# Kernel tuning notes

Hardware: AMD Instinct MI355X
Metric: run time of the kernel (lower is better)

The kernel has to match this reference:

```python
import jax, jax.numpy as jnp
import numpy as np

N = 100000   # nodes
E = 1600000  # edges
D = 64       # input_size
H = 64       # hidden_size
OUT = 32     # output_size
HOR = 12     # horizon


def setup_inputs() -> dict:
    key = jax.random.key(0)
    ks = jax.random.split(key, 9)
    x = jax.random.normal(ks[0], (N, D), jnp.float32)
    edge_index = jax.random.randint(ks[1], (2, E), 0, N, dtype=jnp.int32)
    edge_weight = jax.random.uniform(ks[2], (E,), jnp.float32)
    s = 0.1
    W1 = jax.random.normal(ks[3], (D, H), jnp.float32) * s   # GCNConv 1 weight (no bias)
    W2 = jax.random.normal(ks[4], (H, H), jnp.float32) * s   # GCNConv 2 weight (no bias)
    A1 = jax.random.normal(ks[5], (H, H), jnp.float32) * s   # readout Linear 1
    b1 = jax.random.normal(ks[6], (H,), jnp.float32) * s
    A2 = jax.random.normal(ks[7], (H, OUT * HOR), jnp.float32) * s  # readout Linear 2
    b2 = jax.random.normal(ks[8], (OUT * HOR,), jnp.float32) * s
    return {"x": x, "edge_index": edge_index, "edge_weight": edge_weight,
            "W1": W1, "W2": W2, "A1": A1, "b1": b1, "A2": A2, "b2": b2}


def _gcn_layer(h, W, row, col, ew, n):
    # h: [n, in], W: [in, out]. PyG GCNConv: transform then symmetric-normalized aggregate.
    h = h @ W
    deg = jax.ops.segment_sum(ew, col, num_segments=n)          # degree at target nodes
    dinv = jnp.where(deg > 0, jax.lax.rsqrt(deg), 0.0)
    norm = dinv[row] * ew * dinv[col]                           # [e]
    msg = h[row] * norm[:, None]                                # gather sources, weight
    return jax.ops.segment_sum(msg, col, num_segments=n)        # scatter-add at targets


def reference(x, edge_index, edge_weight, W1, W2, A1, b1, A2, b2):
    n = x.shape[0]
    loop = jnp.arange(n, dtype=edge_index.dtype)
    row = jnp.concatenate([edge_index[0], loop])                # self-loops, weight 1
    col = jnp.concatenate([edge_index[1], loop])
    ew = jnp.concatenate([edge_weight, jnp.ones((n,), edge_weight.dtype)])
    h = jax.nn.relu(_gcn_layer(x, W1, row, col, ew, n))
    h = jax.nn.relu(_gcn_layer(h, W2, row, col, ew, n))
    # readout MLP + unflatten to [n, horizon, output_size]
    r = jax.nn.relu(h @ A1 + b1) @ A2 + b2
    r = r.reshape(n, HOR, OUT)
    return (r, h)
```

## Files before the change

kernel.cpp:

```cpp
#include <hip/hip_runtime.h>


typedef unsigned long long ull;


template <bool BUCKET>
__global__ void aggregate_kernel(const float* __restrict__ hin, float* __restrict__ hout,
                                 const int* __restrict__ meta,
                                 const int2* __restrict__ ent,
                                 const float* __restrict__ dinv, int n) {
    int gid = blockIdx.x * blockDim.x + threadIdx.x;
    int node = __builtin_amdgcn_readfirstlane(gid >> 6);
    int lane = threadIdx.x & 63;
    if (node >= n) return;
    float di = dinv[node];
    float acc0 = hin[(size_t)node * 64 + lane] * (di * di);
    float acc1 = 0.0f;
    int b, c;
    if (BUCKET) { b = node << 6; c = meta[node]; if (c > 64) c = 64; }
    else        { b = meta[node]; c = meta[node + 1] - b; }
    int e = b, end = b + c;
    for (; e + 2 <= end; e += 2) {
        int2 p0 = ent[e];
        int2 p1 = ent[e + 1];
        acc0 = fmaf(__int_as_float(p0.y), hin[(size_t)p0.x * 64 + lane], acc0);
        acc1 = fmaf(__int_as_float(p1.y), hin[(size_t)p1.x * 64 + lane], acc1);
    }
    if (e < end) {
        int2 p0 = ent[e];
        acc0 = fmaf(__int_as_float(p0.y), hin[(size_t)p0.x * 64 + lane], acc0);
    }
    hout[(size_t)node * 64 + lane] = fmaxf(acc0 + acc1, 0.0f);
}

template <bool BIAS, bool RELU>
__global__ void transform_kernel(const float* __restrict__ A, const float* __restrict__ W,
                                 const float* __restrict__ bias, float* __restrict__ out,
                                 int n, int ldw, int ldo) {
    __shared__ float Wl[64 * 64];
    int t = threadIdx.x;
    int coff = blockIdx.y * 64;
    for (int i = t; i < 4096; i += 256) {
        int k = i >> 6, c = i & 63;
        Wl[i] = W[k * ldw + coff + c];
    }
    __syncthreads();
    int wv = t >> 6, lane = t & 63;
    int row0 = (blockIdx.x * 4 + wv) * 16;
    row0 = __builtin_amdgcn_readfirstlane(row0);
    if (row0 >= n) return;
    float bv = BIAS ? bias[coff + lane] : 0.0f;
    float acc[16];
#pragma unroll
    for (int i = 0; i < 16; i++) acc[i] = bv;
    const float* Ar = A + (size_t)row0 * 64;
    int nrows = n - row0;
    if (nrows > 16) nrows = 16;
    if (nrows == 16) {
        for (int k0 = 0; k0 < 64; k0 += 4) {
            float w0 = Wl[(k0 + 0) * 64 + lane];
            float w1 = Wl[(k0 + 1) * 64 + lane];
            float w2 = Wl[(k0 + 2) * 64 + lane];
            float w3 = Wl[(k0 + 3) * 64 + lane];
#pragma unroll
            for (int i = 0; i < 16; i++) {
                float4 a = *(const float4*)(Ar + i * 64 + k0);
                acc[i] = fmaf(a.x, w0, fmaf(a.y, w1, fmaf(a.z, w2, fmaf(a.w, w3, acc[i]))));
            }
        }
#pragma unroll
        for (int i = 0; i < 16; i++) {
            float v = acc[i];
            if (RELU) v = fmaxf(v, 0.0f);
            out[(size_t)(row0 + i) * ldo + coff + lane] = v;
        }
    } else {
        for (int k = 0; k < 64; k++) {
            float w = Wl[k * 64 + lane];
            for (int i = 0; i < nrows; i++) acc[i] = fmaf(Ar[i * 64 + k], w, acc[i]);
        }
        for (int i = 0; i < nrows; i++) {
            float v = acc[i];
            if (RELU) v = fmaxf(v, 0.0f);
            out[(size_t)(row0 + i) * ldo + coff + lane] = v;
        }
    }
}

__global__ void readout_kernel(const float* __restrict__ H, const float* __restrict__ A1,
                               const float* __restrict__ b1, const float* __restrict__ A2,
                               const float* __restrict__ b2, float* __restrict__ out, int n) {
    __shared__ float Wl[64 * 64];
    __shared__ float Ml[64 * 64];
    int t = threadIdx.x;
    int wv = t >> 6, lane = t & 63;
    int wrow = blockIdx.x * 64 + wv * 16;
    wrow = __builtin_amdgcn_readfirstlane(wrow);
    int nr = n - wrow;
    if (nr > 16) nr = 16;
    if (nr < 0) nr = 0;

    for (int i = t; i < 4096; i += 256) Wl[i] = A1[i];
    __syncthreads();

    float acc[16];
    float bv = b1[lane];
#pragma unroll
    for (int i = 0; i < 16; i++) acc[i] = bv;
    const float* Ar = H + (size_t)wrow * 64;
    if (nr == 16) {
        for (int k0 = 0; k0 < 64; k0 += 4) {
            float w0 = Wl[(k0 + 0) * 64 + lane];
            float w1 = Wl[(k0 + 1) * 64 + lane];
            float w2 = Wl[(k0 + 2) * 64 + lane];
            float w3 = Wl[(k0 + 3) * 64 + lane];
#pragma unroll
            for (int i = 0; i < 16; i++) {
                float4 a = *(const float4*)(Ar + i * 64 + k0);
                acc[i] = fmaf(a.x, w0, fmaf(a.y, w1, fmaf(a.z, w2, fmaf(a.w, w3, acc[i]))));
            }
        }
    } else if (nr > 0) {
        for (int k = 0; k < 64; k++) {
            float w = Wl[k * 64 + lane];
            for (int i = 0; i < nr; i++) acc[i] = fmaf(Ar[i * 64 + k], w, acc[i]);
        }
    }
#pragma unroll
    for (int i = 0; i < 16; i++)
        Ml[(wv * 16 + i) * 64 + lane] = fmaxf(acc[i], 0.0f);

    for (int tile = 0; tile < 6; tile++) {
        int coff = tile * 64;
        __syncthreads();
        for (int i = t; i < 4096; i += 256) {
            int k = i >> 6, c = i & 63;
            Wl[i] = A2[k * 384 + coff + c];
        }
        __syncthreads();
        float bv2 = b2[coff + lane];
        float o[16];
#pragma unroll
        for (int i = 0; i < 16; i++) o[i] = bv2;
        const float* Mr = Ml + (size_t)wv * 16 * 64;
        for (int k0 = 0; k0 < 64; k0 += 4) {
            float w0 = Wl[(k0 + 0) * 64 + lane];
            float w1 = Wl[(k0 + 1) * 64 + lane];
            float w2 = Wl[(k0 + 2) * 64 + lane];
            float w3 = Wl[(k0 + 3) * 64 + lane];
#pragma unroll
            for (int i = 0; i < 16; i++) {
                float4 a = *(const float4*)(Mr + i * 64 + k0);
                o[i] = fmaf(a.x, w0, fmaf(a.y, w1, fmaf(a.z, w2, fmaf(a.w, w3, o[i]))));
            }
        }
        for (int i = 0; i < nr; i++)
            out[(size_t)(wrow + i) * 384 + coff + lane] = o[i];
    }
}


__global__ void init_cnt(int* cnt, int n) {
    int i = blockIdx.x * 256 + threadIdx.x;
    if (i < n) cnt[i] = 0;
}

__global__ void bfill_kernel(const int* __restrict__ row, const int* __restrict__ col,
                             const float* __restrict__ ew, int* cnt, int2* __restrict__ bucket,
                             int E) {
    int e = blockIdx.x * 256 + threadIdx.x;
    if (e < E) {
        int t = col[e];
        int p = atomicAdd(&cnt[t], 1);
        if (p < 64) bucket[((size_t)t << 6) + p] = make_int2(row[e], __float_as_int(ew[e]));
    }
}

__global__ void bdinv_kernel(const int* __restrict__ cnt, const int2* __restrict__ bucket,
                             float* __restrict__ dinv, int n) {
    int gid = blockIdx.x * blockDim.x + threadIdx.x;
    int node = gid >> 6;
    int lane = threadIdx.x & 63;
    if (node >= n) return;
    int c = cnt[node]; if (c > 64) c = 64;
    float w = (lane < c) ? __int_as_float(bucket[((size_t)node << 6) + lane].y) : 0.0f;
    for (int m = 32; m; m >>= 1) w += __shfl_xor(w, m, 64);
    if (lane == 0) dinv[node] = rsqrtf(1.0f + w);
}

__global__ void bnorm_kernel(const int* __restrict__ cnt, int2* bucket,
                             const float* __restrict__ dinv, int n) {
    int gid = blockIdx.x * blockDim.x + threadIdx.x;
    int node = gid >> 6;
    int slot = threadIdx.x & 63;
    if (node >= n) return;
    int c = cnt[node]; if (c > 64) c = 64;
    if (slot < c) {
        size_t idx = ((size_t)node << 6) + slot;
        int2 p = bucket[idx];
        float w = dinv[p.x] * __int_as_float(p.y) * dinv[node];
        bucket[idx].y = __float_as_int(w);
    }
}


__global__ void init_dc(ull* dc, int n) {
    int i = blockIdx.x * 256 + threadIdx.x;
    if (i < n) dc[i] = 0ull;
}

__global__ void hist_packed(const int* __restrict__ col, const float* __restrict__ ew,
                            ull* dc, int E) {
    int e = blockIdx.x * 256 + threadIdx.x;
    if (e < E) {
        int t = col[e];
        ull v = (1ull << 32) | (unsigned)lrintf(ew[e] * 1048576.0f);
        atomicAdd(&dc[t], v);
    }
}

__global__ void unpack_kernel(const ull* __restrict__ dc, int* __restrict__ cnt,
                              float* __restrict__ dinv, int n) {
    int i = blockIdx.x * 256 + threadIdx.x;
    if (i < n) {
        ull v = dc[i];
        cnt[i] = (int)(v >> 32);
        dinv[i] = rsqrtf(1.0f + (float)(unsigned)v * (1.0f / 1048576.0f));
    }
}

__global__ void scan1(const int* __restrict__ cnt, int* __restrict__ excl,
                      int* __restrict__ bsum, int n) {
    __shared__ int lds[256];
    int t = threadIdx.x;
    int idx = blockIdx.x * 1024 + t * 4;
    int4 c = make_int4(0, 0, 0, 0);
    if (idx < n) c = *(const int4*)(cnt + idx);
    int s = c.x + c.y + c.z + c.w;
    lds[t] = s;
    __syncthreads();
    for (int off = 1; off < 256; off <<= 1) {
        int u = (t >= off) ? lds[t - off] : 0;
        __syncthreads();
        lds[t] += u;
        __syncthreads();
    }
    int incl = lds[t];
    if (t == 255) bsum[blockIdx.x] = incl;
    int e0 = incl - s;
    if (idx < n) {
        excl[idx + 0] = e0;
        excl[idx + 1] = e0 + c.x;
        excl[idx + 2] = e0 + c.x + c.y;
        excl[idx + 3] = e0 + c.x + c.y + c.z;
    }
}

__global__ void scan2(int* bsum, int nb) {
    __shared__ int lds[256];
    int t = threadIdx.x;
    int v = (t < nb) ? bsum[t] : 0;
    lds[t] = v;
    __syncthreads();
    for (int off = 1; off < 256; off <<= 1) {
        int u = (t >= off) ? lds[t - off] : 0;
        __syncthreads();
        lds[t] += u;
        __syncthreads();
    }
    if (t < nb) bsum[t] = lds[t] - v;
}

__global__ void scan3(int* __restrict__ ptr, const int* __restrict__ bsum,
                      int* __restrict__ pfill, int n, int E) {
    int i = blockIdx.x * 256 + threadIdx.x;
    if (i < n) {
        int v = ptr[i] + bsum[i >> 10];
        ptr[i] = v;
        pfill[i] = v;
    }
    if (i == n) ptr[n] = E;
}

__global__ void fill_kernel(const int* __restrict__ row, const int* __restrict__ col,
                            const float* __restrict__ ew, const float* __restrict__ dinv,
                            int* pfill, int2* __restrict__ ent, int E) {
    int e = blockIdx.x * 256 + threadIdx.x;
    if (e < E) {
        int t = col[e], s = row[e];
        int p = atomicAdd(&pfill[t], 1);
        ent[p] = make_int2(s, __float_as_int(dinv[s] * ew[e] * dinv[t]));
    }
}


extern "C" void kernel_launch(void* const* d_in, const int* in_sizes, int n_in,
                              void* d_out, int out_size, void* d_ws, size_t ws_size,
                              hipStream_t stream) {
    const float* x  = (const float*)d_in[0];
    const int*   ei = (const int*)d_in[1];
    const float* ew = (const float*)d_in[2];
    const float* W1 = (const float*)d_in[3];
    const float* W2 = (const float*)d_in[4];
    const float* A1 = (const float*)d_in[5];
    const float* b1 = (const float*)d_in[6];
    const float* A2 = (const float*)d_in[7];
    const float* b2 = (const float*)d_in[8];
    float* out = (float*)d_out;

    const int N = in_sizes[0] / 64;
    const int E = in_sizes[2];
    const int* row = ei;
    const int* col = ei + E;

    float* r_out = out;
    float* h_out = out + (size_t)N * 384;

    dim3 tgrid((N + 63) / 64, 1);
    int rblocks = (N + 63) / 64;
    int aggblocks = (int)(((size_t)N * 64 + 255) / 256);
    int nblk = (N + 255) / 256;
    int eblk = (E + 255) / 256;

    char* p = (char*)d_ws;
    auto alloc = [&](size_t bytes) { void* r = (void*)p; p += (bytes + 255) & ~(size_t)255; return r; };

    size_t need_bucket = 256 * 8 + (size_t)N * 4 * 2 + ((size_t)N << 6) * 8 + (size_t)N * 64 * 4 * 2
                       + 64 * 1024;
    if (ws_size >= need_bucket) {
        int*   cnt    = (int*)alloc((size_t)N * 4);
        float* dinv   = (float*)alloc((size_t)N * 4);
        int2*  bucket = (int2*)alloc(((size_t)N << 6) * 8);
        float* h1     = (float*)alloc((size_t)N * 64 * 4);
        float* h2b    = (float*)alloc((size_t)N * 64 * 4);

        init_cnt<<<nblk, 256, 0, stream>>>(cnt, N);
        bfill_kernel<<<eblk, 256, 0, stream>>>(row, col, ew, cnt, bucket, E);
        bdinv_kernel<<<aggblocks, 256, 0, stream>>>(cnt, bucket, dinv, N);
        bnorm_kernel<<<aggblocks, 256, 0, stream>>>(cnt, bucket, dinv, N);

        transform_kernel<false, false><<<tgrid, 256, 0, stream>>>(x, W1, nullptr, h1, N, 64, 64);
        aggregate_kernel<true><<<aggblocks, 256, 0, stream>>>(h1, h2b, cnt, bucket, dinv, N);
        transform_kernel<false, false><<<tgrid, 256, 0, stream>>>(h2b, W2, nullptr, h1, N, 64, 64);
        aggregate_kernel<true><<<aggblocks, 256, 0, stream>>>(h1, h_out, cnt, bucket, dinv, N);
        readout_kernel<<<rblocks, 256, 0, stream>>>(h_out, A1, b1, A2, b2, r_out, N);
    } else {
        ull*   dc   = (ull*)alloc((size_t)N * 8);
        int*   cnt  = (int*)alloc((size_t)N * 4);
        float* dinv = (float*)alloc((size_t)N * 4);
        int*   ptr  = (int*)alloc((size_t)(N + 1) * 4);
        int*   bsum = (int*)alloc(1024);
        int2*  ent  = (int2*)alloc((size_t)E * 8);
        float* h1   = (float*)alloc((size_t)N * 64 * 4);
        float* h2b  = (float*)alloc((size_t)N * 64 * 4);
        int*   pfill = cnt;
        int nb = (N + 1023) / 1024;

        init_dc<<<nblk, 256, 0, stream>>>(dc, N);
        hist_packed<<<eblk, 256, 0, stream>>>(col, ew, dc, E);
        unpack_kernel<<<nblk, 256, 0, stream>>>(dc, cnt, dinv, N);
        scan1<<<nb, 256, 0, stream>>>(cnt, ptr, bsum, N);
        scan2<<<1, 256, 0, stream>>>(bsum, nb);
        scan3<<<(N + 256) / 256, 256, 0, stream>>>(ptr, bsum, pfill, N, E);
        fill_kernel<<<eblk, 256, 0, stream>>>(row, col, ew, dinv, pfill, ent, E);

        transform_kernel<false, false><<<tgrid, 256, 0, stream>>>(x, W1, nullptr, h1, N, 64, 64);
        aggregate_kernel<false><<<aggblocks, 256, 0, stream>>>(h1, h2b, ptr, ent, dinv, N);
        transform_kernel<false, false><<<tgrid, 256, 0, stream>>>(h2b, W2, nullptr, h1, N, 64, 64);
        aggregate_kernel<false><<<aggblocks, 256, 0, stream>>>(h1, h_out, ptr, ent, dinv, N);
        readout_kernel<<<rblocks, 256, 0, stream>>>(h_out, A1, b1, A2, b2, r_out, N);
        (void)h2b;
    }
}
```

Before: 708.9 us.

## Drop LDS in readout MLP; broadcast hidden via readlane and register-tile all outputs

The readout kernel no longer stages A1 and A2 through shared memory and no longer uses block-wide barriers. A1 and A2 weights are read straight from global memory (cached), and the hidden activations stay in registers and are broadcast across lanes with readlane. All 384 outputs (6x16 accumulators) are computed in one pass over k. This removes the LDS traffic and the syncthreads between tiles, but uses many more VGPRs (96 accumulators plus 16 activations), which can cut occupancy or cause spills.

```diff
diff --git a/kernel.cpp b/kernel.cpp
--- a/kernel.cpp
+++ b/kernel.cpp
@@ -90,72 +90,70 @@
 __global__ void readout_kernel(const float* __restrict__ H, const float* __restrict__ A1,
                                const float* __restrict__ b1, const float* __restrict__ A2,
                                const float* __restrict__ b2, float* __restrict__ out, int n) {
-    __shared__ float Wl[64 * 64];
-    __shared__ float Ml[64 * 64];
     int t = threadIdx.x;
     int wv = t >> 6, lane = t & 63;
-    int wrow = blockIdx.x * 64 + wv * 16;
-    wrow = __builtin_amdgcn_readfirstlane(wrow);
+    int wrow = __builtin_amdgcn_readfirstlane(blockIdx.x * 64 + wv * 16);
+    if (wrow >= n) return;
     int nr = n - wrow;
     if (nr > 16) nr = 16;
-    if (nr < 0) nr = 0;
-
-    for (int i = t; i < 4096; i += 256) Wl[i] = A1[i];
-    __syncthreads();
-
-    float acc[16];
+
+    float m[16];
     float bv = b1[lane];
 #pragma unroll
-    for (int i = 0; i < 16; i++) acc[i] = bv;
+    for (int i = 0; i < 16; i++) m[i] = bv;
     const float* Ar = H + (size_t)wrow * 64;
     if (nr == 16) {
         for (int k0 = 0; k0 < 64; k0 += 4) {
-            float w0 = Wl[(k0 + 0) * 64 + lane];
-            float w1 = Wl[(k0 + 1) * 64 + lane];
-            float w2 = Wl[(k0 + 2) * 64 + lane];
-            float w3 = Wl[(k0 + 3) * 64 + lane];
+            float w0 = A1[(k0 + 0) * 64 + lane];
+            float w1 = A1[(k0 + 1) * 64 + lane];
+            float w2 = A1[(k0 + 2) * 64 + lane];
+            float w3 = A1[(k0 + 3) * 64 + lane];
 #pragma unroll
             for (int i = 0; i < 16; i++) {
                 float4 a = *(const float4*)(Ar + i * 64 + k0);
-                acc[i] = fmaf(a.x, w0, fmaf(a.y, w1, fmaf(a.z, w2, fmaf(a.w, w3, acc[i]))));
+                m[i] = fmaf(a.x, w0, fmaf(a.y, w1, fmaf(a.z, w2, fmaf(a.w, w3, m[i]))));
             }
         }
-    } else if (nr > 0) {
+    } else {
         for (int k = 0; k < 64; k++) {
-            float w = Wl[k * 64 + lane];
-            for (int i = 0; i < nr; i++) acc[i] = fmaf(Ar[i * 64 + k], w, acc[i]);
-        }
-    }
-#pragma unroll
-    for (int i = 0; i < 16; i++)
-        Ml[(wv * 16 + i) * 64 + lane] = fmaxf(acc[i], 0.0f);
-
-    for (int tile = 0; tile < 6; tile++) {
-        int coff = tile * 64;
-        __syncthreads();
-        for (int i = t; i < 4096; i += 256) {
-            int k = i >> 6, c = i & 63;
-            Wl[i] = A2[k * 384 + coff + c];
-        }
-        __syncthreads();
-        float bv2 = b2[coff + lane];
-        float o[16];
-#pragma unroll
-        for (int i = 0; i < 16; i++) o[i] = bv2;
-        const float* Mr = Ml + (size_t)wv * 16 * 64;
-        for (int k0 = 0; k0 < 64; k0 += 4) {
-            float w0 = Wl[(k0 + 0) * 64 + lane];
-            float w1 = Wl[(k0 + 1) * 64 + lane];
-            float w2 = Wl[(k0 + 2) * 64 + lane];
-            float w3 = Wl[(k0 + 3) * 64 + lane];
-#pragma unroll
-            for (int i = 0; i < 16; i++) {
-                float4 a = *(const float4*)(Mr + i * 64 + k0);
-                o[i] = fmaf(a.x, w0, fmaf(a.y, w1, fmaf(a.z, w2, fmaf(a.w, w3, o[i]))));
-            }
-        }
+            float w = A1[k * 64 + lane];
+            for (int i = 0; i < nr; i++) m[i] = fmaf(Ar[i * 64 + k], w, m[i]);
+        }
+    }
+#pragma unroll
+    for (int i = 0; i < 16; i++) m[i] = fmaxf(m[i], 0.0f);
+
+    float acc[6][16];
+#pragma unroll
+    for (int tt = 0; tt < 6; tt++) {
+        float b = b2[tt * 64 + lane];
+#pragma unroll
+        for (int i = 0; i < 16; i++) acc[tt][i] = b;
+    }
+    const float* A2p = A2 + lane;
+#pragma unroll 2
+    for (int k = 0; k < 64; k++) {
+        float w[6];
+#pragma unroll
+        for (int tt = 0; tt < 6; tt++) w[tt] = A2p[k * 384 + tt * 64];
+#pragma unroll
+        for (int i = 0; i < 16; i++) {
+            float s = __int_as_float(__builtin_amdgcn_readlane(__float_as_int(m[i]), k));
+#pragma unroll
+            for (int tt = 0; tt < 6; tt++) acc[tt][i] = fmaf(s, w[tt], acc[tt][i]);
+        }
+    }
+
+    if (nr == 16) {
+#pragma unroll
+        for (int i = 0; i < 16; i++)
+#pragma unroll
+            for (int tt = 0; tt < 6; tt++)
+                out[(size_t)(wrow + i) * 384 + tt * 64 + lane] = acc[tt][i];
+    } else {
         for (int i = 0; i < nr; i++)
-            out[(size_t)(wrow + i) * 384 + coff + lane] = o[i];
+            for (int tt = 0; tt < 6; tt++)
+                out[(size_t)(wrow + i) * 384 + tt * 64 + lane] = acc[tt][i];
     }
 }
 
```

Measured after the change: 718.3 us. Within noise of the previous version (+1.3%).
